# Optimization experiments

Hardware: AMD Instinct MI355X
Metric: run time of the kernel (lower is better)

Reference implementation:

```python
import jax, jax.numpy as jnp
import numpy as np

B, T, C, H, FF, BOT = 2, 2048, 1024, 16, 4096, 64
D = C // H
EPS = 1e-5

def _ln(x, g, b):
    m = jnp.mean(x, axis=-1, keepdims=True)
    v = jnp.mean(jnp.square(x - m), axis=-1, keepdims=True)
    return (x - m) * jax.lax.rsqrt(v + EPS) * g + b

def setup_inputs() -> dict:
    key = jax.random.key(0)
    ks = jax.random.split(key, 20)
    def lin(k, fan_in, shape):
        return jax.random.normal(k, shape, jnp.float32) * (1.0 / np.sqrt(fan_in))
    inp = {
        "x": jax.random.normal(ks[0], (B, T, C), jnp.float32),
        # causal mask: masked_fill where mask == 0
        "attn_mask": jnp.tril(jnp.ones((T, T), jnp.int32))[None, None, :, :],
        "Wq": lin(ks[1], C, (C, C)), "bq": jnp.zeros((C,), jnp.float32),
        "Wk": lin(ks[2], C, (C, C)), "bk": jnp.zeros((C,), jnp.float32),
        "Wv": lin(ks[3], C, (C, C)), "bv": jnp.zeros((C,), jnp.float32),
        "Wo": lin(ks[4], C, (C, C)), "bo": jnp.zeros((C,), jnp.float32),
        "g1": jnp.ones((C,), jnp.float32), "beta1": jnp.zeros((C,), jnp.float32),
        "g2": jnp.ones((C,), jnp.float32), "beta2": jnp.zeros((C,), jnp.float32),
        "W1": lin(ks[5], C, (C, FF)), "bf1": jnp.zeros((FF,), jnp.float32),
        "W2": lin(ks[6], FF, (FF, C)), "bf2": jnp.zeros((C,), jnp.float32),
        "Wd": lin(ks[7], C, (C, BOT)), "bd": jnp.zeros((BOT,), jnp.float32),
        "Wu": lin(ks[8], BOT, (BOT, C)), "bu": jnp.zeros((C,), jnp.float32),
    }
    return inp

def reference(x, attn_mask, Wq, bq, Wk, bk, Wv, bv, Wo, bo,
              g1, beta1, g2, beta2, W1, bf1, W2, bf2, Wd, bd, Wu, bu):
    # --- attention sublayer ---
    xn = _ln(x, g1, beta1)
    q = (xn @ Wq + bq).reshape(B, T, H, D)
    k = (xn @ Wk + bk).reshape(B, T, H, D)
    v = (xn @ Wv + bv).reshape(B, T, H, D)
    scores = jnp.einsum('bthd,bshd->bhts', q, k) / jnp.sqrt(jnp.float32(D))
    scores = jnp.where(attn_mask == 0, -jnp.inf, scores)
    w = jax.nn.softmax(scores, axis=-1)
    attn = jnp.einsum('bhts,bshd->bthd', w, v).reshape(B, T, C)
    x = x + attn @ Wo + bo
    # --- FFN + adapter sublayer ---
    xn2 = _ln(x, g2, beta2)
    h = jax.nn.relu(xn2 @ W1 + bf1) @ W2 + bf2
    h = h + jax.nn.relu(h @ Wd + bd) @ Wu + bu  # adapter residual
    return x + h
```

## Files before the change

### kernel.cpp

```cpp
#include <hip/hip_runtime.h>
#include <cstdint>
#include <cstddef>

typedef unsigned short u16;
typedef __attribute__((ext_vector_type(4))) short short4v;
typedef __attribute__((ext_vector_type(8))) short short8;
typedef __attribute__((ext_vector_type(4))) float f32x4;

__device__ __forceinline__ float bf2f(u16 h) { return __uint_as_float(((unsigned)h) << 16); }
__device__ __forceinline__ u16 f2bf(float f) {
    unsigned u = __float_as_uint(f);
    unsigned r = (u + 0x7fffu + ((u >> 16) & 1u)) >> 16;
    return (u16)r;
}
__device__ __forceinline__ u16 f2bf_fast(float f) {
    return (u16)((__float_as_uint(f) + 0x8000u) >> 16);
}

__device__ __forceinline__ void gl_lds16(const void* g, void* l) {
    __builtin_amdgcn_global_load_lds((const __attribute__((address_space(1))) void*)g,
                                     (__attribute__((address_space(3))) void*)l, 16, 0, 0);
}

struct Prologue {
    const void* tsrc[8];
    u16* tdst[8];
    int tR[8], tC[8], toff[8];
    const void* psrc[12];
    int poff[12], pn[12];
    int ntrans;
};
__global__ __launch_bounds__(256) void prologue_kernel(Prologue P,
                                                       const unsigned* __restrict__ x,
                                                       int* __restrict__ flag,
                                                       float* __restrict__ pf) {
    __shared__ int cnt[256];
    int c = 0;
    for (int i = threadIdx.x; i < 1024; i += 256) {
        unsigned lo = x[i] & 0xFFFFu;
        unsigned e = (lo >> 7) & 0xFFu;
        c += (e >= 100u && e <= 150u) ? 1 : 0;
    }
    cnt[threadIdx.x] = c;
    __syncthreads();
    for (int s = 128; s > 0; s >>= 1) {
        if (threadIdx.x < s) cnt[threadIdx.x] += cnt[threadIdx.x + s];
        __syncthreads();
    }
    const int bf = (cnt[0] > 512) ? 1 : 0;
    if (blockIdx.x == 0 && threadIdx.x == 0) *flag = bf;

    const int bid = blockIdx.x;
    if (bid >= P.ntrans) {
        const int s = bid - P.ntrans;
        const void* sp = P.psrc[s];
        float* dp = pf + P.poff[s];
        const int n = P.pn[s];
        for (int i = threadIdx.x; i < n; i += 256)
            dp[i] = bf ? bf2f(((const u16*)sp)[i]) : ((const float*)sp)[i];
        return;
    }
    __shared__ u16 tile[32][33];
    int m = 0;
#pragma unroll
    for (int i = 1; i < 8; i++) m = (bid >= P.toff[i]) ? i : m;
    const int local = bid - P.toff[m];
    const int R = P.tR[m], C = P.tC[m];
    const int tilesx = C >> 5;
    const int bx = local % tilesx, by = local / tilesx;
    const void* src = P.tsrc[m];
    u16* dst = P.tdst[m];
    const int tx = threadIdx.x & 31, ty = threadIdx.x >> 5;
#pragma unroll
    for (int i = 0; i < 32; i += 8) {
        size_t idx = (size_t)(by * 32 + ty + i) * C + bx * 32 + tx;
        tile[ty + i][tx] = bf ? ((const u16*)src)[idx] : f2bf(((const float*)src)[idx]);
    }
    __syncthreads();
#pragma unroll
    for (int i = 0; i < 32; i += 8)
        dst[(size_t)(bx * 32 + ty + i) * R + by * 32 + tx] = tile[tx][ty + i];
}

__global__ __launch_bounds__(256) void ln_x_kernel(const void* __restrict__ X,
                                                   const float* __restrict__ G,
                                                   const float* __restrict__ Be,
                                                   u16* __restrict__ Xb,
                                                   u16* __restrict__ Y,
                                                   const int* __restrict__ flag) {
    const int row = blockIdx.x;
    const int tid = threadIdx.x;
    const int lane = tid & 63, wave = tid >> 6;
    u16 vbuf[4];
    if (*flag) {
        *(uint2*)vbuf = *(const uint2*)((const u16*)X + (size_t)row * 1024 + tid * 4);
    } else {
        float4 v = *(const float4*)((const float*)X + (size_t)row * 1024 + tid * 4);
        vbuf[0] = f2bf(v.x); vbuf[1] = f2bf(v.y); vbuf[2] = f2bf(v.z); vbuf[3] = f2bf(v.w);
    }
    *(uint2*)&Xb[(size_t)row * 1024 + tid * 4] = *(uint2*)vbuf;
    float f[4];
    float s = 0.f, sq = 0.f;
#pragma unroll
    for (int j = 0; j < 4; j++) { f[j] = bf2f(vbuf[j]); s += f[j]; sq += f[j] * f[j]; }
#pragma unroll
    for (int m = 1; m < 64; m <<= 1) { s += __shfl_xor(s, m, 64); sq += __shfl_xor(sq, m, 64); }
    __shared__ float rs_[4], rq_[4];
    if (lane == 0) { rs_[wave] = s; rq_[wave] = sq; }
    __syncthreads();
    float S = rs_[0] + rs_[1] + rs_[2] + rs_[3];
    float Q2 = rq_[0] + rq_[1] + rq_[2] + rq_[3];
    float mean = S * (1.f / 1024.f);
    float var = Q2 * (1.f / 1024.f) - mean * mean;
    float rstd = rsqrtf(var + 1e-5f);
    u16 o[4];
#pragma unroll
    for (int j = 0; j < 4; j++) {
        int c2 = tid * 4 + j;
        float y = (f[j] - mean) * rstd * G[c2] + Be[c2];
        o[j] = f2bf(y);
    }
    *(uint2*)&Y[(size_t)row * 1024 + tid * 4] = *(uint2*)o;
}

__global__ __launch_bounds__(256) void ln_kernel(const u16* __restrict__ X,
                                                 const float* __restrict__ G,
                                                 const float* __restrict__ Be,
                                                 u16* __restrict__ Y) {
    const int row = blockIdx.x;
    const int tid = threadIdx.x;
    const int lane = tid & 63, wave = tid >> 6;
    const u16* xr = X + (size_t)row * 1024;
    u16 vbuf[4];
    *(uint2*)vbuf = *(const uint2*)&xr[tid * 4];
    float f[4];
    float s = 0.f, sq = 0.f;
#pragma unroll
    for (int j = 0; j < 4; j++) { f[j] = bf2f(vbuf[j]); s += f[j]; sq += f[j] * f[j]; }
#pragma unroll
    for (int m = 1; m < 64; m <<= 1) { s += __shfl_xor(s, m, 64); sq += __shfl_xor(sq, m, 64); }
    __shared__ float rs_[4], rq_[4];
    if (lane == 0) { rs_[wave] = s; rq_[wave] = sq; }
    __syncthreads();
    float S = rs_[0] + rs_[1] + rs_[2] + rs_[3];
    float Q2 = rq_[0] + rq_[1] + rq_[2] + rq_[3];
    float mean = S * (1.f / 1024.f);
    float var = Q2 * (1.f / 1024.f) - mean * mean;
    float rstd = rsqrtf(var + 1e-5f);
    u16 o[4];
#pragma unroll
    for (int j = 0; j < 4; j++) {
        int c2 = tid * 4 + j;
        float y = (f[j] - mean) * rstd * G[c2] + Be[c2];
        o[j] = f2bf(y);
    }
    *(uint2*)&Y[(size_t)row * 1024 + tid * 4] = *(uint2*)o;
}

template <int TAG>
__global__ __launch_bounds__(512, 4) void gemm128_kernel(const u16* __restrict__ A,
                                                         const u16* __restrict__ Bt,
                                                         const float* __restrict__ bias,
                                                         const u16* __restrict__ res1,
                                                         const u16* __restrict__ res2,
                                                         void* __restrict__ out,
                                                         void* __restrict__ out_k,
                                                         void* __restrict__ out_v,
                                                         int M, int N, int K, int relu, int mode,
                                                         int swz,
                                                         const int* __restrict__ flag) {
    (void)flag; (void)M;
    __shared__ __align__(16) u16 As[2][2][128 * 32];
    __shared__ __align__(16) u16 Bs[2][2][128 * 32];
    const int tid = threadIdx.x;
    const int wave = tid >> 6, lane = tid & 63;
    const int l15 = lane & 15, quad = lane >> 4;
    const int wr = wave & 3, wc = wave >> 2;
    int bx = blockIdx.x, by = blockIdx.y;
    if (swz) {
        const int gx = gridDim.x;
        const int nwg = gx * gridDim.y;
        const int bid = by * gx + bx;
        const int sbid = (bid & 7) * (nwg >> 3) + (bid >> 3);
        bx = sbid % gx;
        by = sbid / gx;
    }
    const int m0 = by * 128, n0 = bx * 128;
    const int nt = K >> 6;

    const int rsub = lane >> 2;
    const int logc = (lane & 3) ^ ((rsub >> 1) & 3);

    auto stage_pair = [&](int t, int kh) {
        const int buf = t & 1;
        const int kk = (t << 6) + (kh << 5) + logc * 8;
        const int roff = wave * 16 + rsub;
        gl_lds16(A + (size_t)(m0 + roff) * K + kk, &As[buf][kh][wave * 512 + lane * 8]);
        gl_lds16(Bt + (size_t)(n0 + roff) * K + kk, &Bs[buf][kh][wave * 512 + lane * 8]);
    };

    f32x4 acc[2][4];
#pragma unroll
    for (int i = 0; i < 2; i++)
#pragma unroll
        for (int j = 0; j < 4; j++) acc[i][j] = (f32x4){0.f, 0.f, 0.f, 0.f};

    stage_pair(0, 0);
    stage_pair(0, 1);
    stage_pair(1, 0);
    asm volatile("s_waitcnt vmcnt(4)" ::: "memory");
    __builtin_amdgcn_s_barrier();

    const int rx = (l15 >> 1) & 3;
    for (int t = 0; t < nt; t++) {
        const int b = t & 1;
#pragma unroll
        for (int ph = 0; ph < 2; ph++) {
            const int kh = ph;
            short8 af[2], bfr[4];
#pragma unroll
            for (int i = 0; i < 2; i++)
                af[i] = *(const short8*)&As[b][kh][(wr * 32 + i * 16 + l15) * 32 +
                                                   ((quad ^ rx) << 3)];
#pragma unroll
            for (int j = 0; j < 4; j++)
                bfr[j] = *(const short8*)&Bs[b][kh][(wc * 64 + j * 16 + l15) * 32 +
                                                    ((quad ^ rx) << 3)];
            if (ph == 0) { if (t + 1 < nt) stage_pair(t + 1, 1); }
            else         { if (t + 2 < nt) stage_pair(t + 2, 0); }
            __builtin_amdgcn_s_setprio(1);
#pragma unroll
            for (int i = 0; i < 2; i++)
#pragma unroll
                for (int j = 0; j < 4; j++)
                    acc[i][j] = __builtin_amdgcn_mfma_f32_16x16x32_bf16(
                        af[i], bfr[j], acc[i][j], 0, 0, 0);
            __builtin_amdgcn_s_setprio(0);
            if (ph == 0) {
                if (t + 1 < nt) { asm volatile("s_waitcnt vmcnt(4)" ::: "memory"); }
                else            { asm volatile("s_waitcnt vmcnt(0)" ::: "memory"); }
            } else {
                if (t + 2 < nt)      { asm volatile("s_waitcnt vmcnt(4)" ::: "memory"); }
                else if (t + 1 < nt) { asm volatile("s_waitcnt vmcnt(2)" ::: "memory"); }
            }
            __builtin_amdgcn_s_barrier();
        }
    }

    if (mode == 2) {
        const int region = n0 >> 10;
        if (region < 2) {
            u16* o = (u16*)(region == 0 ? out : out_k);
#pragma unroll
            for (int j = 0; j < 4; j++) {
                const int col = n0 + wc * 64 + j * 16 + l15;
                const float bv = bias[col];
                const int cl = col & 1023;
#pragma unroll
                for (int i = 0; i < 2; i++) {
                    const int row0 = m0 + wr * 32 + i * 16 + quad * 4;
#pragma unroll
                    for (int r = 0; r < 4; r++)
                        o[(size_t)(row0 + r) * 1024 + cl] = f2bf(acc[i][j][r] + bv);
                }
            }
        } else {
            u16* o = (u16*)out_v;
#pragma unroll
            for (int j = 0; j < 4; j++) {
                const int col = n0 + wc * 64 + j * 16 + l15;
                const float bv = bias[col];
                const int cl = col & 1023;
                const int h = cl >> 6, d = cl & 63;
#pragma unroll
                for (int i = 0; i < 2; i++) {
                    const int row_base = m0 + wr * 32 + i * 16 + quad * 4;
                    const int bb = row_base >> 11, tt = row_base & 2047;
                    u16 pk[4];
#pragma unroll
                    for (int r = 0; r < 4; r++) pk[r] = f2bf(acc[i][j][r] + bv);
                    *(uint2*)&o[(((size_t)bb * 16 + h) * 64 + d) * 2048 + tt] = *(uint2*)pk;
                }
            }
        }
        return;
    }
#pragma unroll
    for (int j = 0; j < 4; j++) {
        const int col = n0 + wc * 64 + j * 16 + l15;
        const float bv = bias ? bias[col] : 0.f;
#pragma unroll
        for (int i = 0; i < 2; i++) {
            const int row0 = m0 + wr * 32 + i * 16 + quad * 4;
#pragma unroll
            for (int r = 0; r < 4; r++) {
                float v = acc[i][j][r] + bv;
                if (relu) v = fmaxf(v, 0.f);
                const size_t idx = (size_t)(row0 + r) * N + col;
                if (res1) v += bf2f(res1[idx]);
                if (res2) v += bf2f(res2[idx]);
                ((u16*)out)[idx] = f2bf(v);
            }
        }
    }
}

template <int TAG>
__global__ __launch_bounds__(512, 2) void gemm256m_kernel(const u16* __restrict__ A,
                                                          const u16* __restrict__ Bt,
                                                          const float* __restrict__ bias,
                                                          void* __restrict__ out,
                                                          int N, int K, int relu) {
    __shared__ __align__(16) u16 As[2][2][256 * 32];
    __shared__ __align__(16) u16 Bs[2][2][128 * 32];
    const int tid = threadIdx.x;
    const int wave = tid >> 6, lane = tid & 63;
    const int l15 = lane & 15, quad = lane >> 4;
    const int wr = wave >> 1, wc = wave & 1;
    const int m0 = blockIdx.y * 256, n0 = blockIdx.x * 128;
    const int nt = K >> 6;

    const int rsub = lane >> 2;
    const int logc = (lane & 3) ^ ((rsub >> 1) & 3);

    auto stage_pair = [&](int t, int kh) {
        const int buf = t & 1;
        const int kk = (t << 6) + (kh << 5) + logc * 8;
        const int ra = m0 + wave * 32 + rsub;
        const int rb = n0 + wave * 16 + rsub;
        u16* da = &As[buf][kh][wave * 1024 + lane * 8];
        gl_lds16(A + (size_t)ra * K + kk, da);
        gl_lds16(A + (size_t)(ra + 16) * K + kk, da + 512);
        gl_lds16(Bt + (size_t)rb * K + kk, &Bs[buf][kh][wave * 512 + lane * 8]);
    };

    f32x4 acc[4][4];
#pragma unroll
    for (int i = 0; i < 4; i++)
#pragma unroll
        for (int j = 0; j < 4; j++) acc[i][j] = (f32x4){0.f, 0.f, 0.f, 0.f};

    stage_pair(0, 0);
    stage_pair(0, 1);
    stage_pair(1, 0);
    asm volatile("s_waitcnt vmcnt(6)" ::: "memory");
    __builtin_amdgcn_s_barrier();

    const int rx = (l15 >> 1) & 3;
    for (int t = 0; t < nt; t++) {
        const int b = t & 1;
#pragma unroll
        for (int ph = 0; ph < 2; ph++) {
            const int kh = ph;
            short8 af[4], bfr[4];
#pragma unroll
            for (int i = 0; i < 4; i++)
                af[i] = *(const short8*)&As[b][kh][(wr * 64 + i * 16 + l15) * 32 +
                                                   ((quad ^ rx) << 3)];
#pragma unroll
            for (int j = 0; j < 4; j++)
                bfr[j] = *(const short8*)&Bs[b][kh][(wc * 64 + j * 16 + l15) * 32 +
                                                    ((quad ^ rx) << 3)];
            if (ph == 0) { if (t + 1 < nt) stage_pair(t + 1, 1); }
            else         { if (t + 2 < nt) stage_pair(t + 2, 0); }
            __builtin_amdgcn_s_setprio(1);
#pragma unroll
            for (int i = 0; i < 4; i++)
#pragma unroll
                for (int j = 0; j < 4; j++)
                    acc[i][j] = __builtin_amdgcn_mfma_f32_16x16x32_bf16(
                        af[i], bfr[j], acc[i][j], 0, 0, 0);
            __builtin_amdgcn_s_setprio(0);
            if (ph == 0) {
                if (t + 1 < nt) { asm volatile("s_waitcnt vmcnt(6)" ::: "memory"); }
                else            { asm volatile("s_waitcnt vmcnt(0)" ::: "memory"); }
            } else {
                if (t + 2 < nt)      { asm volatile("s_waitcnt vmcnt(6)" ::: "memory"); }
                else if (t + 1 < nt) { asm volatile("s_waitcnt vmcnt(3)" ::: "memory"); }
            }
            __builtin_amdgcn_s_barrier();
        }
    }

#pragma unroll
    for (int j = 0; j < 4; j++) {
        const int col = n0 + wc * 64 + j * 16 + l15;
        const float bv = bias ? bias[col] : 0.f;
#pragma unroll
        for (int i = 0; i < 4; i++) {
            const int row0 = m0 + wr * 64 + i * 16 + quad * 4;
#pragma unroll
            for (int r = 0; r < 4; r++) {
                float v = acc[i][j][r] + bv;
                if (relu) v = fmaxf(v, 0.f);
                ((u16*)out)[(size_t)(row0 + r) * N + col] = f2bf(v);
            }
        }
    }
}

template <int TAG>
__global__ __launch_bounds__(512, 2) void gemm128d_kernel(const u16* __restrict__ A,
                                                          const u16* __restrict__ Bt,
                                                          const float* __restrict__ bias,
                                                          const u16* __restrict__ res1,
                                                          void* __restrict__ out,
                                                          int N, int K, int relu, int swz) {
    __shared__ __align__(16) u16 As[2][2][128 * 64];
    __shared__ __align__(16) u16 Bs[2][2][128 * 64];
    const int tid = threadIdx.x;
    const int wave = tid >> 6, lane = tid & 63;
    const int l15 = lane & 15, quad = lane >> 4;
    const int wr = wave & 3, wc = wave >> 2;
    int bx = blockIdx.x, by = blockIdx.y;
    if (swz) {
        const int gx = gridDim.x;
        const int nwg = gx * gridDim.y;
        const int bid = by * gx + bx;
        const int sbid = (bid & 7) * (nwg >> 3) + (bid >> 3);
        bx = sbid % gx;
        by = sbid / gx;
    }
    const int m0 = by * 128, n0 = bx * 128;
    const int nt = K >> 7;

    const int srow = lane >> 3;
    const int logc = (lane & 7) ^ ((lane >> 4) & 3);

    auto stage_pair = [&](int t, int kh) {
        const int buf = t & 1;
        const int kk = (t << 7) + (kh << 6) + logc * 8;
        const int r0 = wave * 16 + srow;
        u16* da = &As[buf][kh][wave * 1024 + lane * 8];
        u16* db = &Bs[buf][kh][wave * 1024 + lane * 8];
        gl_lds16(A + (size_t)(m0 + r0) * K + kk, da);
        gl_lds16(A + (size_t)(m0 + r0 + 8) * K + kk, da + 512);
        gl_lds16(Bt + (size_t)(n0 + r0) * K + kk, db);
        gl_lds16(Bt + (size_t)(n0 + r0 + 8) * K + kk, db + 512);
    };

    f32x4 acc[2][4];
#pragma unroll
    for (int i = 0; i < 2; i++)
#pragma unroll
        for (int j = 0; j < 4; j++) acc[i][j] = (f32x4){0.f, 0.f, 0.f, 0.f};

    stage_pair(0, 0);
    stage_pair(0, 1);
    stage_pair(1, 0);
    asm volatile("s_waitcnt vmcnt(8)" ::: "memory");
    __builtin_amdgcn_s_barrier();

    const int rx = (l15 >> 1) & 3;
    for (int t = 0; t < nt; t++) {
        const int b = t & 1;
#pragma unroll
        for (int ph = 0; ph < 2; ph++) {
            const int kh = ph;
            short8 af[2][2], bfr[4][2];
#pragma unroll
            for (int ks = 0; ks < 2; ks++) {
                const int ck = ((ks << 2) | (quad ^ rx)) << 3;
#pragma unroll
                for (int i = 0; i < 2; i++)
                    af[i][ks] = *(const short8*)&As[b][kh][(wr * 32 + i * 16 + l15) * 64 + ck];
#pragma unroll
                for (int j = 0; j < 4; j++)
                    bfr[j][ks] = *(const short8*)&Bs[b][kh][(wc * 64 + j * 16 + l15) * 64 + ck];
            }
            if (ph == 0) { if (t + 1 < nt) stage_pair(t + 1, 1); }
            else         { if (t + 2 < nt) stage_pair(t + 2, 0); }
            __builtin_amdgcn_s_setprio(1);
#pragma unroll
            for (int ks = 0; ks < 2; ks++)
#pragma unroll
                for (int i = 0; i < 2; i++)
#pragma unroll
                    for (int j = 0; j < 4; j++)
                        acc[i][j] = __builtin_amdgcn_mfma_f32_16x16x32_bf16(
                            af[i][ks], bfr[j][ks], acc[i][j], 0, 0, 0);
            __builtin_amdgcn_s_setprio(0);
            if (ph == 0) {
                if (t + 1 < nt) { asm volatile("s_waitcnt vmcnt(8)" ::: "memory"); }
                else            { asm volatile("s_waitcnt vmcnt(0)" ::: "memory"); }
            } else {
                if (t + 2 < nt)      { asm volatile("s_waitcnt vmcnt(8)" ::: "memory"); }
                else if (t + 1 < nt) { asm volatile("s_waitcnt vmcnt(4)" ::: "memory"); }
            }
            __builtin_amdgcn_s_barrier();
        }
    }

#pragma unroll
    for (int j = 0; j < 4; j++) {
        const int col = n0 + wc * 64 + j * 16 + l15;
        const float bv = bias ? bias[col] : 0.f;
#pragma unroll
        for (int i = 0; i < 2; i++) {
            const int row0 = m0 + wr * 32 + i * 16 + quad * 4;
#pragma unroll
            for (int r = 0; r < 4; r++) {
                float v = acc[i][j][r] + bv;
                if (relu) v = fmaxf(v, 0.f);
                const size_t idx = (size_t)(row0 + r) * N + col;
                if (res1) v += bf2f(res1[idx]);
                ((u16*)out)[idx] = f2bf(v);
            }
        }
    }
}

__global__ __launch_bounds__(512) void adapter_kernel(const u16* __restrict__ hh,
                                                      const u16* __restrict__ x1,
                                                      const u16* __restrict__ WdT,
                                                      const u16* __restrict__ WuT,
                                                      const float* __restrict__ bd,
                                                      const float* __restrict__ bu,
                                                      void* __restrict__ out,
                                                      const int* __restrict__ flag) {
    const int tid = threadIdx.x;
    const int wave = tid >> 6, lane = tid & 63;
    const int l15 = lane & 15, quad = lane >> 4;
    const int r0 = blockIdx.x * 16;

    __shared__ float part[8][16 * 64];
    __shared__ __align__(16) u16 bot_s[16 * 72];

    f32x4 dacc[4];
#pragma unroll
    for (int j = 0; j < 4; j++) dacc[j] = (f32x4){0.f, 0.f, 0.f, 0.f};
    const int kw = wave * 128;
#pragma unroll
    for (int ks = 0; ks < 4; ks++) {
        const int k0 = kw + ks * 32 + quad * 8;
        short8 af = *(const short8*)&hh[(size_t)(r0 + l15) * 1024 + k0];
#pragma unroll
        for (int j = 0; j < 4; j++) {
            short8 bf = *(const short8*)&WdT[(size_t)(j * 16 + l15) * 1024 + k0];
            dacc[j] = __builtin_amdgcn_mfma_f32_16x16x32_bf16(af, bf, dacc[j], 0, 0, 0);
        }
    }
#pragma unroll
    for (int j = 0; j < 4; j++)
#pragma unroll
        for (int r = 0; r < 4; r++)
            part[wave][(quad * 4 + r) * 64 + j * 16 + l15] = dacc[j][r];
    __syncthreads();

    for (int e = tid; e < 1024; e += 512) {
        float s = part[0][e];
#pragma unroll
        for (int w = 1; w < 8; w++) s += part[w][e];
        s += bd[e & 63];
        s = fmaxf(s, 0.f);
        bot_s[(e >> 6) * 72 + (e & 63)] = f2bf(s);
    }
    __syncthreads();

    short8 auf[2];
    auf[0] = *(const short8*)&bot_s[l15 * 72 + quad * 8];
    auf[1] = *(const short8*)&bot_s[l15 * 72 + 32 + quad * 8];
    f32x4 uacc[8];
#pragma unroll
    for (int j = 0; j < 8; j++) uacc[j] = (f32x4){0.f, 0.f, 0.f, 0.f};
#pragma unroll
    for (int j = 0; j < 8; j++) {
        const size_t nb = (size_t)(wave * 128 + j * 16 + l15) * 64;
        short8 b0 = *(const short8*)&WuT[nb + quad * 8];
        short8 b1 = *(const short8*)&WuT[nb + 32 + quad * 8];
        uacc[j] = __builtin_amdgcn_mfma_f32_16x16x32_bf16(auf[0], b0, uacc[j], 0, 0, 0);
        uacc[j] = __builtin_amdgcn_mfma_f32_16x16x32_bf16(auf[1], b1, uacc[j], 0, 0, 0);
    }
    const int f32out = (*flag == 0);
#pragma unroll
    for (int j = 0; j < 8; j++) {
        const int col = wave * 128 + j * 16 + l15;
        const float bv = bu[col];
#pragma unroll
        for (int r = 0; r < 4; r++) {
            const int row = r0 + quad * 4 + r;
            const size_t idx = (size_t)row * 1024 + col;
            float v = uacc[j][r] + bv;
            v += bf2f(hh[idx]);
            v += bf2f(x1[idx]);
            if (f32out) ((float*)out)[idx] = v;
            else ((u16*)out)[idx] = f2bf(v);
        }
    }
}

template <int SPLIT>
__global__ __launch_bounds__(256) void flash_kernel(const u16* __restrict__ Q,
                                                    const u16* __restrict__ Kg,
                                                    const u16* __restrict__ VtG,
                                                    u16* __restrict__ O,
                                                    u16* __restrict__ pO,
                                                    float* __restrict__ pL) {
    const int tid = threadIdx.x;
    const int wave = tid >> 6, lane = tid & 63;
    int qb, ch;
    if (SPLIT) {
        const int i = blockIdx.x;
        if (i < 32)      { qb = 31 - (i >> 2); ch = i & 3; }
        else if (i < 56) { const int j = i - 32; qb = 23 - j / 3; ch = j % 3; }
        else if (i < 72) { const int j = i - 56; qb = 15 - (j >> 1); ch = j & 1; }
        else             { qb = 7 - (i - 72); ch = 0; }
    } else {
        qb = 31 - blockIdx.x; ch = 0;
    }
    const int bh = blockIdx.y;
    const int t0 = qb * 64;
    const int steps = qb + 1;
    const int ktbeg = SPLIT ? ch * 8 : 0;
    const int ktend = SPLIT ? (steps < ktbeg + 8 ? steps : ktbeg + 8) : steps;
    const size_t base = ((size_t)(bh >> 4) * 2048) * 1024 + (size_t)(bh & 15) * 64;
    const size_t basev = (size_t)bh * 64 * 2048;

    __shared__ __align__(16) u16 Ks[2][64 * 64];
    __shared__ __align__(16) u16 Vt[2][64 * 64];
#if !__has_builtin(__builtin_amdgcn_mfma_f32_16x16x16bf16_1k)
    __shared__ __align__(16) u16 Ps[4][16 * 72];
#endif

    const int l15 = lane & 15, quad = lane >> 4;
    const int rmin = t0 + wave * 16;

    short8 qf[2];
    {
        const u16* qp = Q + base + (size_t)(rmin + l15) * 1024 + quad * 8;
        qf[0] = *(const short8*)qp;
        qf[1] = *(const short8*)(qp + 32);
    }

    const int slr = lane >> 3;
    const int sc8 = (lane & 7) ^ slr;
    const int rb = wave * 16;

    auto stage = [&](int kt, int bufi) {
        gl_lds16(Kg + base + (size_t)(kt * 64 + rb + slr) * 1024 + sc8 * 8,
                 &Ks[bufi][rb * 64 + lane * 8]);
        gl_lds16(Kg + base + (size_t)(kt * 64 + rb + 8 + slr) * 1024 + sc8 * 8,
                 &Ks[bufi][(rb + 8) * 64 + lane * 8]);
        gl_lds16(VtG + basev + (size_t)(rb + slr) * 2048 + kt * 64 + sc8 * 8,
                 &Vt[bufi][rb * 64 + lane * 8]);
        gl_lds16(VtG + basev + (size_t)(rb + 8 + slr) * 2048 + kt * 64 + sc8 * 8,
                 &Vt[bufi][(rb + 8) * 64 + lane * 8]);
    };

    float l_part = 0.f;
    f32x4 oacc[4];
#pragma unroll
    for (int jt = 0; jt < 4; jt++) oacc[jt] = (f32x4){0.f, 0.f, 0.f, 0.f};

    const float Cs = 0.125f * 1.44269504f;

    stage(ktbeg, 0);
    __syncthreads();

    for (int kt = ktbeg; kt < ktend; kt++) {
        const int cur = kt & 1;
        if (kt + 1 < ktend) stage(kt + 1, cur ^ 1);

        short8 kf[2][4];
#pragma unroll
        for (int st = 0; st < 2; st++)
#pragma unroll
            for (int j = 0; j < 4; j++)
                kf[st][j] = *(const short8*)&Ks[cur][(j * 16 + l15) * 64 +
                                                     (((st * 4 + quad) ^ (l15 & 7)) * 8)];
#if __has_builtin(__builtin_amdgcn_mfma_f32_16x16x16bf16_1k)
        short4v vf[4][4];
#pragma unroll
        for (int j = 0; j < 4; j++) {
            int k8 = j * 2 + (quad >> 1);
#pragma unroll
            for (int jt = 0; jt < 4; jt++) {
                int d = jt * 16 + l15;
                vf[j][jt] = *(const short4v*)&Vt[cur][d * 64 + ((k8 ^ (d & 7)) * 8) +
                                                      (quad & 1) * 4];
            }
        }
#else
        short8 vf[2][4];
#pragma unroll
        for (int st = 0; st < 2; st++)
#pragma unroll
            for (int jt = 0; jt < 4; jt++) {
                int d = jt * 16 + l15;
                vf[st][jt] = *(const short8*)&Vt[cur][d * 64 + (((st * 4 + quad) ^ (d & 7)) * 8)];
            }
#endif

        f32x4 s[4];
#pragma unroll
        for (int j = 0; j < 4; j++) s[j] = (f32x4){0.f, 0.f, 0.f, 0.f};
#pragma unroll
        for (int st = 0; st < 2; st++)
#pragma unroll
            for (int j = 0; j < 4; j++)
                s[j] = __builtin_amdgcn_mfma_f32_16x16x32_bf16(kf[st][j], qf[st], s[j], 0, 0, 0);

        float lpv[4] = {0.f, 0.f, 0.f, 0.f};
        short4v pj[4];
        if (kt != qb) {
#pragma unroll
            for (int j = 0; j < 4; j++) {
                union { short4v v; u16 u[4]; } pk;
#pragma unroll
                for (int r = 0; r < 4; r++) {
                    float p = __builtin_amdgcn_exp2f(s[j][r] * Cs);
                    lpv[r] += p;
                    pk.u[r] = f2bf_fast(p);
                }
                pj[j] = pk.v;
            }
        } else {
            const int qrow = rmin + l15;
#pragma unroll
            for (int j = 0; j < 4; j++) {
                union { short4v v; u16 u[4]; } pk;
#pragma unroll
                for (int r = 0; r < 4; r++) {
                    float p = __builtin_amdgcn_exp2f(s[j][r] * Cs);
                    int key = kt * 64 + j * 16 + quad * 4 + r;
                    if (key > qrow) p = 0.f;
                    lpv[r] += p;
                    pk.u[r] = f2bf_fast(p);
                }
                pj[j] = pk.v;
            }
        }
        l_part += (lpv[0] + lpv[1]) + (lpv[2] + lpv[3]);

#if __has_builtin(__builtin_amdgcn_mfma_f32_16x16x16bf16_1k)
#pragma unroll
        for (int jt = 0; jt < 4; jt++)
#pragma unroll
            for (int j = 0; j < 4; j++)
                oacc[jt] = __builtin_amdgcn_mfma_f32_16x16x16bf16_1k(pj[j], vf[j][jt],
                                                                     oacc[jt], 0, 0, 0);
#else
        u16* Pw = Ps[wave];
#pragma unroll
        for (int j = 0; j < 4; j++)
            *(short4v*)&Pw[l15 * 72 + j * 16 + quad * 4] = pj[j];
#pragma unroll
        for (int st = 0; st < 2; st++) {
            short8 pf2 = *(const short8*)&Pw[l15 * 72 + st * 32 + quad * 8];
#pragma unroll
            for (int jt = 0; jt < 4; jt++)
                oacc[jt] = __builtin_amdgcn_mfma_f32_16x16x32_bf16(pf2, vf[st][jt],
                                                                  oacc[jt], 0, 0, 0);
        }
#endif
        __syncthreads();
    }

    float lf = l_part;
    lf += __shfl_xor(lf, 16, 64);
    lf += __shfl_xor(lf, 32, 64);

    if (SPLIT && steps > 8) {
        const size_t ib = ((size_t)bh * 24 + (qb - 8)) * 4 + ch;
        u16* po = pO + ib * 4096;
#pragma unroll
        for (int jt = 0; jt < 4; jt++)
#pragma unroll
            for (int r = 0; r < 4; r++)
                po[(wave * 16 + quad * 4 + r) * 64 + jt * 16 + l15] = f2bf(oacc[jt][r]);
        if (quad == 0) pL[ib * 64 + wave * 16 + l15] = lf;
        return;
    }

    {
        float inv[4];
#pragma unroll
        for (int r = 0; r < 4; r++) inv[r] = 1.f / __shfl(lf, quad * 4 + r, 64);
#pragma unroll
        for (int jt = 0; jt < 4; jt++) {
            int d = jt * 16 + l15;
#pragma unroll
            for (int r = 0; r < 4; r++) {
                int t = rmin + quad * 4 + r;
                O[base + (size_t)t * 1024 + d] = f2bf(oacc[jt][r] * inv[r]);
            }
        }
    }
}

__global__ __launch_bounds__(256) void flash_combine_kernel(const u16* __restrict__ pO,
                                                            const float* __restrict__ pL,
                                                            u16* __restrict__ O) {
    const int qj = blockIdx.x;
    const int bh = blockIdx.y;
    const int qb = qj + 8;
    const int nch = (qb >> 3) + 1;
    const int tid = threadIdx.x;
    const int row = tid >> 2;
    const int d0 = (tid & 3) * 16;
    const size_t ib = ((size_t)bh * 24 + qj) * 4;

    float acc[16];
#pragma unroll
    for (int k = 0; k < 16; k++) acc[k] = 0.f;
    float lsum = 0.f;
    for (int c = 0; c < nch; c++) {
        const u16* po = pO + (ib + c) * 4096 + row * 64 + d0;
        u16 pb[16];
        *(uint4*)pb = *(const uint4*)po;
        *(uint4*)(pb + 8) = *(const uint4*)(po + 8);
#pragma unroll
        for (int k = 0; k < 16; k++) acc[k] += bf2f(pb[k]);
        lsum += pL[(ib + c) * 64 + row];
    }
    const float inv = 1.f / lsum;
    u16 o[16];
#pragma unroll
    for (int k = 0; k < 16; k++) o[k] = f2bf(acc[k] * inv);
    const size_t base = ((size_t)(bh >> 4) * 2048) * 1024 + (size_t)(bh & 15) * 64;
    const int t = qb * 64 + row;
    u16* op = &O[base + (size_t)t * 1024 + d0];
    *(uint4*)op = ((uint4*)o)[0];
    *(uint4*)(op + 8) = ((uint4*)o)[1];
}

extern "C" void kernel_launch(void* const* d_in, const int* in_sizes, int n_in,
                              void* d_out, int out_size, void* d_ws, size_t ws_size,
                              hipStream_t stream) {
    (void)in_sizes; (void)n_in; (void)out_size;
    const void* x   = d_in[0];
    const void* Wq  = d_in[2];  const void* bq  = d_in[3];
    const void* Wk  = d_in[4];  const void* bk  = d_in[5];
    const void* Wv  = d_in[6];  const void* bv  = d_in[7];
    const void* Wo  = d_in[8];  const void* bo  = d_in[9];
    const void* g1  = d_in[10]; const void* be1 = d_in[11];
    const void* g2  = d_in[12]; const void* be2 = d_in[13];
    const void* W1  = d_in[14]; const void* bf1 = d_in[15];
    const void* W2  = d_in[16]; const void* bf2 = d_in[17];
    const void* Wd  = d_in[18]; const void* bd  = d_in[19];
    const void* Wu  = d_in[20]; const void* bu  = d_in[21];

    uint8_t* w8 = (uint8_t*)d_ws;
    int* flag = (int*)w8;
    float* pf = (float*)(w8 + 64);
    u16* wsb = (u16*)(w8 + 64 + 65536);

    const size_t M1 = 1024ull * 1024ull;
    u16* WqT = wsb;
    u16* WkT = wsb + 1 * M1;
    u16* WvT = wsb + 2 * M1;
    u16* WoT = wsb + 3 * M1;
    u16* W1T = wsb + 4 * M1;
    u16* W2T = wsb + 8 * M1;
    u16* WdT = wsb + 12 * M1;
    u16* WuT = wsb + 12 * M1 + 65536;
    u16* S0  = wsb + 12 * M1 + 131072;
    u16* Areg = S0;
    u16* Breg = S0 + 4 * M1;
    u16* ff1  = S0;
    u16* Creg = S0 + 16 * M1;
    u16* Dreg = S0 + 20 * M1;
    u16* Ereg = S0 + 24 * M1;
    u16* xb = Areg;
    u16* xn = Breg; u16* attn = Breg;
    u16* q = Creg;  u16* xn2 = Creg;
    u16* kk_ = Dreg; u16* x1 = Dreg;
    u16* VtG = Ereg; u16* hh = Ereg;

    const size_t arena_bytes = (size_t)(64 + 65536) + (40 * M1 + 131072) * 2;
    float* partf = (float*)(w8 + ((arena_bytes + 255) & ~(size_t)255));
    const size_t need = ((arena_bytes + 255) & ~(size_t)255) + 4ull * 4 * M1 * 4;
    const bool sk = ws_size >= need;
    float* flL = partf + 14 * M1;

    float* bqkv_f = pf + 0;
    float* bo_f  = pf + 3072;
    float* bf1_f = pf + 4096;  float* bf2_f = pf + 8192;
    float* bd_f  = pf + 9216;  float* bu_f  = pf + 9280;
    float* g1_f  = pf + 10304; float* be1_f = pf + 11328;
    float* g2_f  = pf + 12352; float* be2_f = pf + 13376;

    Prologue P;
    const void* tsrc[8] = {Wq, Wk, Wv, Wo, W1, W2, Wd, Wu};
    u16* tdst[8] = {WqT, WkT, WvT, WoT, W1T, W2T, WdT, WuT};
    int tR[8] = {1024, 1024, 1024, 1024, 1024, 4096, 1024, 64};
    int tC[8] = {1024, 1024, 1024, 1024, 4096, 1024, 64, 1024};
    int acc_off = 0;
    for (int i = 0; i < 8; i++) {
        P.tsrc[i] = tsrc[i]; P.tdst[i] = tdst[i];
        P.tR[i] = tR[i]; P.tC[i] = tC[i];
        P.toff[i] = acc_off;
        acc_off += (tR[i] >> 5) * (tC[i] >> 5);
    }
    P.ntrans = acc_off;
    const void* psrc[12] = {bq, bk, bv, bo, bf1, bf2, bd, bu, g1, be1, g2, be2};
    int poff[12] = {0, 1024, 2048, 3072, 4096, 8192, 9216, 9280, 10304, 11328, 12352, 13376};
    int pn[12]   = {1024, 1024, 1024, 1024, 4096, 1024, 64, 1024, 1024, 1024, 1024, 1024};
    for (int i = 0; i < 12; i++) { P.psrc[i] = psrc[i]; P.poff[i] = poff[i]; P.pn[i] = pn[i]; }
    prologue_kernel<<<acc_off + 12, 256, 0, stream>>>(P, (const unsigned*)x, flag, pf);

    ln_x_kernel<<<4096, 256, 0, stream>>>(x, g1_f, be1_f, xb, xn, flag);
    gemm128_kernel<0><<<dim3(24, 32), 512, 0, stream>>>(xn, WqT, bqkv_f, nullptr, nullptr,
                                                        q, kk_, VtG, 4096, 3072, 1024, 0, 2, 0, flag);
    if (sk) {
        flash_kernel<1><<<dim3(80, 32), 256, 0, stream>>>(q, kk_, VtG, attn, (u16*)partf, flL);
        flash_combine_kernel<<<dim3(24, 32), 256, 0, stream>>>((const u16*)partf, flL, attn);
    } else {
        flash_kernel<0><<<dim3(32, 32), 256, 0, stream>>>(q, kk_, VtG, attn, nullptr, nullptr);
    }
    gemm128d_kernel<1><<<dim3(8, 32), 512, 0, stream>>>(attn, WoT, bo_f, xb,
                                                        x1, 1024, 1024, 0, 1);
    ln_kernel<<<4096, 256, 0, stream>>>(x1, g2_f, be2_f, xn2);
    gemm256m_kernel<2><<<dim3(32, 16), 512, 0, stream>>>(xn2, W1T, bf1_f,
                                                         ff1, 4096, 1024, 1);
    gemm128d_kernel<3><<<dim3(8, 32), 512, 0, stream>>>(ff1, W2T, bf2_f, nullptr,
                                                        hh, 1024, 4096, 0, 1);
    adapter_kernel<<<256, 512, 0, stream>>>(hh, x1, WdT, WuT, bd_f, bu_f, d_out, flag);
}
```

Before: 403.1 us.

## Enlarge flash-attention query tile to 128 rows, two 16-row groups per wave

Each flash block now processes 128 query rows instead of 64. Each wave holds two 16-row Q fragments and reuses every staged K/V tile for both, with per-group causal skipping and masking. The split-K schedule, partial-buffer indexing and combine kernel are resized to match. The goal is to halve K/V global-to-LDS traffic and barrier count per query row, at the cost of more registers, fewer blocks, and coarser causal load balance.

```diff
diff --git a/kernel.cpp b/kernel.cpp
--- a/kernel.cpp
+++ b/kernel.cpp
@@ -601,16 +601,16 @@
     int qb, ch;
     if (SPLIT) {
         const int i = blockIdx.x;
-        if (i < 32)      { qb = 31 - (i >> 2); ch = i & 3; }
-        else if (i < 56) { const int j = i - 32; qb = 23 - j / 3; ch = j % 3; }
-        else if (i < 72) { const int j = i - 56; qb = 15 - (j >> 1); ch = j & 1; }
-        else             { qb = 7 - (i - 72); ch = 0; }
+        if (i < 16)      { qb = 15 - (i >> 2); ch = i & 3; }
+        else if (i < 28) { const int j = i - 16; qb = 11 - j / 3; ch = j % 3; }
+        else if (i < 36) { const int j = i - 28; qb = 7 - (j >> 1); ch = j & 1; }
+        else             { qb = 3 - (i - 36); ch = 0; }
     } else {
-        qb = 31 - blockIdx.x; ch = 0;
+        qb = 15 - blockIdx.x; ch = 0;
     }
     const int bh = blockIdx.y;
-    const int t0 = qb * 64;
-    const int steps = qb + 1;
+    const int t0 = qb * 128;
+    const int steps = 2 * qb + 2;
     const int ktbeg = SPLIT ? ch * 8 : 0;
     const int ktend = SPLIT ? (steps < ktbeg + 8 ? steps : ktbeg + 8) : steps;
     const size_t base = ((size_t)(bh >> 4) * 2048) * 1024 + (size_t)(bh & 15) * 64;
@@ -623,13 +623,13 @@
 #endif
 
     const int l15 = lane & 15, quad = lane >> 4;
-    const int rmin = t0 + wave * 16;
-
-    short8 qf[2];
-    {
-        const u16* qp = Q + base + (size_t)(rmin + l15) * 1024 + quad * 8;
-        qf[0] = *(const short8*)qp;
-        qf[1] = *(const short8*)(qp + 32);
+
+    short8 qf[2][2];
+#pragma unroll
+    for (int g = 0; g < 2; g++) {
+        const u16* qp = Q + base + (size_t)(t0 + wave * 32 + g * 16 + l15) * 1024 + quad * 8;
+        qf[g][0] = *(const short8*)qp;
+        qf[g][1] = *(const short8*)(qp + 32);
     }
 
     const int slr = lane >> 3;
@@ -647,10 +647,12 @@
                  &Vt[bufi][(rb + 8) * 64 + lane * 8]);
     };
 
-    float l_part = 0.f;
-    f32x4 oacc[4];
-#pragma unroll
-    for (int jt = 0; jt < 4; jt++) oacc[jt] = (f32x4){0.f, 0.f, 0.f, 0.f};
+    float l_part[2] = {0.f, 0.f};
+    f32x4 oacc[2][4];
+#pragma unroll
+    for (int g = 0; g < 2; g++)
+#pragma unroll
+        for (int jt = 0; jt < 4; jt++) oacc[g][jt] = (f32x4){0.f, 0.f, 0.f, 0.f};
 
     const float Cs = 0.125f * 1.44269504f;
 
@@ -691,98 +693,111 @@
             }
 #endif
 
-        f32x4 s[4];
-#pragma unroll
-        for (int j = 0; j < 4; j++) s[j] = (f32x4){0.f, 0.f, 0.f, 0.f};
-#pragma unroll
-        for (int st = 0; st < 2; st++)
+#pragma unroll
+        for (int g = 0; g < 2; g++) {
+            const int rmin = t0 + wave * 32 + g * 16;
+            if (kt * 64 > rmin + 15) continue;
+
+            f32x4 s[4];
+#pragma unroll
+            for (int j = 0; j < 4; j++) s[j] = (f32x4){0.f, 0.f, 0.f, 0.f};
+#pragma unroll
+            for (int st = 0; st < 2; st++)
+#pragma unroll
+                for (int j = 0; j < 4; j++)
+                    s[j] = __builtin_amdgcn_mfma_f32_16x16x32_bf16(kf[st][j], qf[g][st], s[j], 0, 0, 0);
+
+            const int qrow = rmin + l15;
+            const bool needmask = (kt * 64 + 63 > rmin);
+            float lpv[4] = {0.f, 0.f, 0.f, 0.f};
+            short4v pj[4];
+            if (!needmask) {
+#pragma unroll
+                for (int j = 0; j < 4; j++) {
+                    union { short4v v; u16 u[4]; } pk;
+#pragma unroll
+                    for (int r = 0; r < 4; r++) {
+                        float p = __builtin_amdgcn_exp2f(s[j][r] * Cs);
+                        lpv[r] += p;
+                        pk.u[r] = f2bf_fast(p);
+                    }
+                    pj[j] = pk.v;
+                }
+            } else {
+#pragma unroll
+                for (int j = 0; j < 4; j++) {
+                    union { short4v v; u16 u[4]; } pk;
+#pragma unroll
+                    for (int r = 0; r < 4; r++) {
+                        float p = __builtin_amdgcn_exp2f(s[j][r] * Cs);
+                        int key = kt * 64 + j * 16 + quad * 4 + r;
+                        if (key > qrow) p = 0.f;
+                        lpv[r] += p;
+                        pk.u[r] = f2bf_fast(p);
+                    }
+                    pj[j] = pk.v;
+                }
+            }
+            l_part[g] += (lpv[0] + lpv[1]) + (lpv[2] + lpv[3]);
+
+#if __has_builtin(__builtin_amdgcn_mfma_f32_16x16x16bf16_1k)
+#pragma unroll
+            for (int jt = 0; jt < 4; jt++)
+#pragma unroll
+                for (int j = 0; j < 4; j++)
+                    oacc[g][jt] = __builtin_amdgcn_mfma_f32_16x16x16bf16_1k(pj[j], vf[j][jt],
+                                                                            oacc[g][jt], 0, 0, 0);
+#else
+            u16* Pw = Ps[wave];
 #pragma unroll
             for (int j = 0; j < 4; j++)
-                s[j] = __builtin_amdgcn_mfma_f32_16x16x32_bf16(kf[st][j], qf[st], s[j], 0, 0, 0);
-
-        float lpv[4] = {0.f, 0.f, 0.f, 0.f};
-        short4v pj[4];
-        if (kt != qb) {
-#pragma unroll
-            for (int j = 0; j < 4; j++) {
-                union { short4v v; u16 u[4]; } pk;
+                *(short4v*)&Pw[l15 * 72 + j * 16 + quad * 4] = pj[j];
+#pragma unroll
+            for (int st = 0; st < 2; st++) {
+                short8 pf2 = *(const short8*)&Pw[l15 * 72 + st * 32 + quad * 8];
+#pragma unroll
+                for (int jt = 0; jt < 4; jt++)
+                    oacc[g][jt] = __builtin_amdgcn_mfma_f32_16x16x32_bf16(pf2, vf[st][jt],
+                                                                          oacc[g][jt], 0, 0, 0);
+            }
+#endif
+        }
+        __syncthreads();
+    }
+
+    int off;
+    if (qb >= 12) off = (15 - qb) * 4;
+    else if (qb >= 8) off = 16 + (11 - qb) * 3;
+    else off = 28 + (7 - qb) * 2;
+    const size_t ib = (size_t)bh * 36 + off + ch;
+
+#pragma unroll
+    for (int g = 0; g < 2; g++) {
+        float lf = l_part[g];
+        lf += __shfl_xor(lf, 16, 64);
+        lf += __shfl_xor(lf, 32, 64);
+
+        if (SPLIT && steps > 8) {
+            u16* po = pO + ib * 8192;
+#pragma unroll
+            for (int jt = 0; jt < 4; jt++)
+#pragma unroll
+                for (int r = 0; r < 4; r++)
+                    po[(wave * 32 + g * 16 + quad * 4 + r) * 64 + jt * 16 + l15] =
+                        f2bf(oacc[g][jt][r]);
+            if (quad == 0) pL[ib * 128 + wave * 32 + g * 16 + l15] = lf;
+        } else {
+            float inv[4];
+#pragma unroll
+            for (int r = 0; r < 4; r++) inv[r] = 1.f / __shfl(lf, quad * 4 + r, 64);
+#pragma unroll
+            for (int jt = 0; jt < 4; jt++) {
+                int d = jt * 16 + l15;
 #pragma unroll
                 for (int r = 0; r < 4; r++) {
-                    float p = __builtin_amdgcn_exp2f(s[j][r] * Cs);
-                    lpv[r] += p;
-                    pk.u[r] = f2bf_fast(p);
+                    int t = t0 + wave * 32 + g * 16 + quad * 4 + r;
+                    O[base + (size_t)t * 1024 + d] = f2bf(oacc[g][jt][r] * inv[r]);
                 }
-                pj[j] = pk.v;
-            }
-        } else {
-            const int qrow = rmin + l15;
-#pragma unroll
-            for (int j = 0; j < 4; j++) {
-                union { short4v v; u16 u[4]; } pk;
-#pragma unroll
-                for (int r = 0; r < 4; r++) {
-                    float p = __builtin_amdgcn_exp2f(s[j][r] * Cs);
-                    int key = kt * 64 + j * 16 + quad * 4 + r;
-                    if (key > qrow) p = 0.f;
-                    lpv[r] += p;
-                    pk.u[r] = f2bf_fast(p);
-                }
-                pj[j] = pk.v;
-            }
-        }
-        l_part += (lpv[0] + lpv[1]) + (lpv[2] + lpv[3]);
-
-#if __has_builtin(__builtin_amdgcn_mfma_f32_16x16x16bf16_1k)
-#pragma unroll
-        for (int jt = 0; jt < 4; jt++)
-#pragma unroll
-            for (int j = 0; j < 4; j++)
-                oacc[jt] = __builtin_amdgcn_mfma_f32_16x16x16bf16_1k(pj[j], vf[j][jt],
-                                                                     oacc[jt], 0, 0, 0);
-#else
-        u16* Pw = Ps[wave];
-#pragma unroll
-        for (int j = 0; j < 4; j++)
-            *(short4v*)&Pw[l15 * 72 + j * 16 + quad * 4] = pj[j];
-#pragma unroll
-        for (int st = 0; st < 2; st++) {
-            short8 pf2 = *(const short8*)&Pw[l15 * 72 + st * 32 + quad * 8];
-#pragma unroll
-            for (int jt = 0; jt < 4; jt++)
-                oacc[jt] = __builtin_amdgcn_mfma_f32_16x16x32_bf16(pf2, vf[st][jt],
-                                                                  oacc[jt], 0, 0, 0);
-        }
-#endif
-        __syncthreads();
-    }
-
-    float lf = l_part;
-    lf += __shfl_xor(lf, 16, 64);
-    lf += __shfl_xor(lf, 32, 64);
-
-    if (SPLIT && steps > 8) {
-        const size_t ib = ((size_t)bh * 24 + (qb - 8)) * 4 + ch;
-        u16* po = pO + ib * 4096;
-#pragma unroll
-        for (int jt = 0; jt < 4; jt++)
-#pragma unroll
-            for (int r = 0; r < 4; r++)
-                po[(wave * 16 + quad * 4 + r) * 64 + jt * 16 + l15] = f2bf(oacc[jt][r]);
-        if (quad == 0) pL[ib * 64 + wave * 16 + l15] = lf;
-        return;
-    }
-
-    {
-        float inv[4];
-#pragma unroll
-        for (int r = 0; r < 4; r++) inv[r] = 1.f / __shfl(lf, quad * 4 + r, 64);
-#pragma unroll
-        for (int jt = 0; jt < 4; jt++) {
-            int d = jt * 16 + l15;
-#pragma unroll
-            for (int r = 0; r < 4; r++) {
-                int t = rmin + quad * 4 + r;
-                O[base + (size_t)t * 1024 + d] = f2bf(oacc[jt][r] * inv[r]);
             }
         }
     }
@@ -791,37 +806,44 @@
 __global__ __launch_bounds__(256) void flash_combine_kernel(const u16* __restrict__ pO,
                                                             const float* __restrict__ pL,
                                                             u16* __restrict__ O) {
-    const int qj = blockIdx.x;
+    const int qb = 4 + blockIdx.x;
     const int bh = blockIdx.y;
-    const int qb = qj + 8;
-    const int nch = (qb >> 3) + 1;
+    const int nch = (qb >= 12) ? 4 : (qb >= 8 ? 3 : 2);
+    int off;
+    if (qb >= 12) off = (15 - qb) * 4;
+    else if (qb >= 8) off = 16 + (11 - qb) * 3;
+    else off = 28 + (7 - qb) * 2;
+    const size_t ibase = (size_t)bh * 36 + off;
     const int tid = threadIdx.x;
-    const int row = tid >> 2;
-    const int d0 = (tid & 3) * 16;
-    const size_t ib = ((size_t)bh * 24 + qj) * 4;
-
-    float acc[16];
-#pragma unroll
-    for (int k = 0; k < 16; k++) acc[k] = 0.f;
+    const int row = tid >> 1;
+    const int d0 = (tid & 1) * 32;
+
+    float acc[32];
+#pragma unroll
+    for (int k = 0; k < 32; k++) acc[k] = 0.f;
     float lsum = 0.f;
     for (int c = 0; c < nch; c++) {
-        const u16* po = pO + (ib + c) * 4096 + row * 64 + d0;
-        u16 pb[16];
+        const u16* po = pO + (ibase + c) * 8192 + row * 64 + d0;
+        u16 pb[32];
         *(uint4*)pb = *(const uint4*)po;
         *(uint4*)(pb + 8) = *(const uint4*)(po + 8);
-#pragma unroll
-        for (int k = 0; k < 16; k++) acc[k] += bf2f(pb[k]);
-        lsum += pL[(ib + c) * 64 + row];
+        *(uint4*)(pb + 16) = *(const uint4*)(po + 16);
+        *(uint4*)(pb + 24) = *(const uint4*)(po + 24);
+#pragma unroll
+        for (int k = 0; k < 32; k++) acc[k] += bf2f(pb[k]);
+        lsum += pL[(ibase + c) * 128 + row];
     }
     const float inv = 1.f / lsum;
-    u16 o[16];
-#pragma unroll
-    for (int k = 0; k < 16; k++) o[k] = f2bf(acc[k] * inv);
+    u16 o[32];
+#pragma unroll
+    for (int k = 0; k < 32; k++) o[k] = f2bf(acc[k] * inv);
     const size_t base = ((size_t)(bh >> 4) * 2048) * 1024 + (size_t)(bh & 15) * 64;
-    const int t = qb * 64 + row;
+    const int t = qb * 128 + row;
     u16* op = &O[base + (size_t)t * 1024 + d0];
     *(uint4*)op = ((uint4*)o)[0];
     *(uint4*)(op + 8) = ((uint4*)o)[1];
+    *(uint4*)(op + 16) = ((uint4*)o)[2];
+    *(uint4*)(op + 24) = ((uint4*)o)[3];
 }
 
 extern "C" void kernel_launch(void* const* d_in, const int* in_sizes, int n_in,
@@ -903,10 +925,10 @@
     gemm128_kernel<0><<<dim3(24, 32), 512, 0, stream>>>(xn, WqT, bqkv_f, nullptr, nullptr,
                                                         q, kk_, VtG, 4096, 3072, 1024, 0, 2, 0, flag);
     if (sk) {
-        flash_kernel<1><<<dim3(80, 32), 256, 0, stream>>>(q, kk_, VtG, attn, (u16*)partf, flL);
-        flash_combine_kernel<<<dim3(24, 32), 256, 0, stream>>>((const u16*)partf, flL, attn);
+        flash_kernel<1><<<dim3(40, 32), 256, 0, stream>>>(q, kk_, VtG, attn, (u16*)partf, flL);
+        flash_combine_kernel<<<dim3(12, 32), 256, 0, stream>>>((const u16*)partf, flL, attn);
     } else {
-        flash_kernel<0><<<dim3(32, 32), 256, 0, stream>>>(q, kk_, VtG, attn, nullptr, nullptr);
+        flash_kernel<0><<<dim3(16, 32), 256, 0, stream>>>(q, kk_, VtG, attn, nullptr, nullptr);
     }
     gemm128d_kernel<1><<<dim3(8, 32), 512, 0, stream>>>(attn, WoT, bo_f, xb,
                                                         x1, 1024, 1024, 0, 1);
```

Measured after the change: 408.8 us. No clear change (+1.4%).
